# Kernel tuning notes

Measured on AMD Instinct MI355X. Metric: run time of the kernel, lower is better.

The kernel has to match this reference:

```python
import jax, jax.numpy as jnp
import numpy as np

B, L, H, NH, P = 4, 1024, 1024, 16, 2048
HD = H // NH


def setup_inputs() -> dict:
    key = jax.random.key(0)
    ks = jax.random.split(key, 6)
    x = jax.random.normal(ks[0], (B, L, H), dtype=jnp.float32)
    # torch.nn.Linear weights are [out, in]
    Wqkv = jax.random.normal(ks[1], (3 * H, H), dtype=jnp.float32) * 0.02
    bqkv = jnp.zeros((3 * H,), dtype=jnp.float32)
    Wo = jax.random.normal(ks[2], (H, H), dtype=jnp.float32) * 0.02
    bo = jnp.zeros((H,), dtype=jnp.float32)
    Er = jax.random.normal(ks[3], (NH, P, HD), dtype=jnp.float32)
    # causal mask: True where attention is disallowed (masked_fill semantics)
    mask = jnp.triu(jnp.ones((L, L), dtype=bool), k=1)
    return {"x": x, "mask": mask, "Wqkv": Wqkv, "bqkv": bqkv,
            "Wo": Wo, "bo": bo, "Er": Er}


def reference(x, mask, Wqkv, bqkv, Wo, bo, Er):
    b, l, d = x.shape
    nh, p, hd = Er.shape
    qkv = x @ Wqkv.T + bqkv                      # [b, l, 3d]
    q, k, v = jnp.split(qkv, 3, axis=-1)
    q = q.reshape(b, l, nh, hd).transpose(0, 2, 1, 3)   # [b, nh, l, hd]
    k = k.reshape(b, l, nh, hd).transpose(0, 2, 1, 3)
    v = v.reshape(b, l, nh, hd).transpose(0, 2, 1, 3)

    scores = jnp.einsum('bnlh,bnkh->bnlk', q, k) / jnp.sqrt(
        jnp.asarray(hd, dtype=x.dtype))

    # relative positions (j - i), torch negative-index wraparound -> mod p
    pos = jnp.arange(l)
    rel = (pos[None, :] - pos[:, None]) % p      # [l, l] in [0, p)
    # Equivalent to einsum('bnlh,rnlkh->bnlk', q, Er[:, rel][None]) but
    # computed as q @ Er^T over all positions then gathered (same math,
    # avoids materializing the [nh, l, l, hd] tensor).
    QEr_full = jnp.einsum('bnlh,nph->bnlp', q, Er)       # [b, nh, l, p]
    i_idx = pos[:, None]                          # broadcasts with rel
    QEr = QEr_full[:, :, i_idx, rel]              # [b, nh, l, l]

    a = scores + QEr
    a = jnp.where(mask, -jnp.inf, a)
    a = jax.nn.softmax(a, axis=-1)                # dropout: eval mode (identity)

    out = jnp.einsum('bnlk,bnkh->bnlh', a, v)     # [b, nh, l, hd]
    out = out.transpose(0, 2, 1, 3).reshape(b, l, d)
    return out @ Wo.T + bo
```

## Files before the change

### kernel.cpp

```cpp
#include <hip/hip_runtime.h>

typedef unsigned short u16;
typedef __bf16 bf16x8 __attribute__((ext_vector_type(8)));
typedef unsigned short u16x8 __attribute__((ext_vector_type(8)));
typedef unsigned short u16x4 __attribute__((ext_vector_type(4)));
typedef float f32x4 __attribute__((ext_vector_type(4)));

#define MFMA16(a, b, c) __builtin_amdgcn_mfma_f32_16x16x32_bf16((a), (b), (c), 0, 0, 0)

#define WAVE_LDS_FENCE() do { \
  asm volatile("s_waitcnt lgkmcnt(0)" ::: "memory"); \
  __builtin_amdgcn_sched_barrier(0); \
} while (0)

#define PIPE_WAIT(N) do { \
  asm volatile("s_waitcnt vmcnt(" #N ")" ::: "memory"); \
  __builtin_amdgcn_sched_barrier(0); \
  __builtin_amdgcn_s_barrier(); \
  __builtin_amdgcn_sched_barrier(0); \
} while (0)

#define GLDS(gp, lp) __builtin_amdgcn_global_load_lds( \
    (const __attribute__((address_space(1))) unsigned int*)(gp), \
    (__attribute__((address_space(3))) unsigned int*)(lp), 16, 0, 0)

__device__ __forceinline__ u16 f2b(float f) {
  unsigned u = __float_as_uint(f);
  u += 0x7fffu + ((u >> 16) & 1u);
  return (u16)(u >> 16);
}
__device__ __forceinline__ float b2f(u16 h) {
  return __uint_as_float(((unsigned)h) << 16);
}

__global__ void cvt_all(const float* __restrict__ x, u16* __restrict__ xb,
                        const float* __restrict__ w1, u16* __restrict__ w1b,
                        const float* __restrict__ w2, u16* __restrict__ w2b) {
  int i = blockIdx.x * blockDim.x + threadIdx.x;
  const float* s; u16* d; int off;
  if (i < 1048576)      { s = x;  d = xb;  off = i; }
  else if (i < 1835008) { s = w1; d = w1b; off = i - 1048576; }
  else                  { s = w2; d = w2b; off = i - 1835008; }
  float4 v = *(const float4*)(s + (size_t)off * 4);
  *(ushort4*)(d + (size_t)off * 4) = make_ushort4(f2b(v.x), f2b(v.y), f2b(v.z), f2b(v.w));
}

__global__ void build_F(const float* __restrict__ Er, u16* __restrict__ Fb) {
  int i = blockIdx.x * blockDim.x + threadIdx.x;
  int base = i * 4;
  int d = base & 63;
  int m = (base >> 6) & 1023;
  int n = base >> 16;
  int sm = (2048 - m) & 2047;
  float4 v = *(const float4*)(Er + ((size_t)(n * 2048 + sm) * 64 + d));
  *(ushort4*)(Fb + (size_t)base) = make_ushort4(f2b(v.x), f2b(v.y), f2b(v.z), f2b(v.w));
}

__global__ __launch_bounds__(256) void transpose_v(const u16* __restrict__ V, u16* __restrict__ Vt) {
  __shared__ u16 T[4096];
  const int bn = blockIdx.x, i0 = blockIdx.y * 64;
  const int t = threadIdx.x;
#pragma unroll
  for (int s = 0; s < 2; ++s) {
    int ch = t + 256 * s;
    int i = ch >> 3, c = ch & 7;
    u16x8 v = *(const u16x8*)&V[(size_t)((bn << 10) + i0 + i) * 64 + c * 8];
#pragma unroll
    for (int e = 0; e < 8; ++e) {
      int d = c * 8 + e;
      T[d * 64 + ((((i >> 3) ^ (d & 7) ^ ((d >> 3) & 7)) & 7) << 3) + (i & 7)] = v[e];
    }
  }
  __syncthreads();
#pragma unroll
  for (int s = 0; s < 2; ++s) {
    int ch = t + 256 * s;
    int d = ch >> 3, cc = ch & 7;
    u16x8 o = *(const u16x8*)&T[d * 64 + (((cc ^ (d & 7) ^ ((d >> 3) & 7)) & 7) << 3)];
    *(u16x8*)&Vt[(size_t)((bn << 6) + d) * 1024 + i0 + cc * 8] = o;
  }
}

__global__ __launch_bounds__(256) void gemm_qkv(const u16* __restrict__ A, const u16* __restrict__ Bw,
                                                const float* __restrict__ bias,
                                                u16* __restrict__ Qo, u16* __restrict__ Ko,
                                                u16* __restrict__ Vo) {
  __shared__ u16 As[3][4][128][8];
  __shared__ u16 Bs[3][4][128][8];
  const int orig = blockIdx.y * 24 + blockIdx.x;
  const int xcd = orig & 7, q = orig >> 3;
  const int mt = ((xcd >> 1) << 3) + q / 12;
  const int nt = (xcd & 1) * 12 + q % 12;
  const int m0 = mt * 128, n0 = nt * 128;
  const int t = threadIdx.x, lane = t & 63, w = t >> 6;
  const int wr = w >> 1, wc = w & 1;
  const int l16 = lane & 15, lg = lane >> 4;
  f32x4 acc[4][4] = {};
  const int r0 = t & 127, g0 = t >> 7;
  const int g1 = g0 + 2;

#define STAGE(buf, k0) do { \
    GLDS(&A[(size_t)(m0 + r0) * 1024 + (k0) + g0 * 8], &As[buf][g0][r0][0]); \
    GLDS(&A[(size_t)(m0 + r0) * 1024 + (k0) + g1 * 8], &As[buf][g1][r0][0]); \
    GLDS(&Bw[(size_t)(n0 + r0) * 1024 + (k0) + g0 * 8], &Bs[buf][g0][r0][0]); \
    GLDS(&Bw[(size_t)(n0 + r0) * 1024 + (k0) + g1 * 8], &Bs[buf][g1][r0][0]); \
  } while (0)

  STAGE(0, 0);
  STAGE(1, 32);

  int buf = 0;
  for (int kt = 0; kt < 32; ++kt) {
    if (kt < 31) PIPE_WAIT(4); else PIPE_WAIT(0);
    if (kt < 30) {
      int nb = buf + 2; if (nb >= 3) nb -= 3;
      STAGE(nb, (kt + 2) * 32);
      __builtin_amdgcn_sched_barrier(0);
    }
    bf16x8 af[4], bfr[4];
#pragma unroll
    for (int m = 0; m < 4; ++m) af[m] = *(const bf16x8*)&As[buf][lg][wr * 64 + m * 16 + l16][0];
#pragma unroll
    for (int n = 0; n < 4; ++n) bfr[n] = *(const bf16x8*)&Bs[buf][lg][wc * 64 + n * 16 + l16][0];
#pragma unroll
    for (int m = 0; m < 4; ++m)
#pragma unroll
      for (int n = 0; n < 4; ++n) acc[m][n] = MFMA16(af[m], bfr[n], acc[m][n]);
    if (++buf == 3) buf = 0;
  }
#undef STAGE

#pragma unroll
  for (int n = 0; n < 4; ++n) {
    int col = n0 + wc * 64 + n * 16 + l16;
    float bq = bias[col];
    int which = col >> 10;
    int h = col & 1023;
    int head = h >> 6, d = h & 63;
    u16* dst = which == 0 ? Qo : (which == 1 ? Ko : Vo);
    float scale = which == 1 ? 0.125f : 1.0f;
#pragma unroll
    for (int m = 0; m < 4; ++m) {
#pragma unroll
      for (int r = 0; r < 4; ++r) {
        int row = m0 + wr * 64 + m * 16 + lg * 4 + r;
        int b = row >> 10, ii = row & 1023;
        float v = (acc[m][n][r] + bq) * scale;
        dst[(size_t)(((b * 16 + head) << 10) + ii) * 64 + d] = f2b(v);
      }
    }
  }
}

__global__ __launch_bounds__(256) void gemm_out(const u16* __restrict__ A, const u16* __restrict__ Bw,
                                                const float* __restrict__ bias, float* __restrict__ Co) {
  __shared__ u16 As[3][4][128][8];
  __shared__ u16 Bs[3][4][128][8];
  const int orig = blockIdx.y * 8 + blockIdx.x;
  const int xcd = orig & 7, q = orig >> 3;
  const int mt = (xcd << 2) + (q >> 3);
  const int nt = q & 7;
  const int m0 = mt * 128, n0 = nt * 128;
  const int t = threadIdx.x, lane = t & 63, w = t >> 6;
  const int wr = w >> 1, wc = w & 1;
  const int l16 = lane & 15, lg = lane >> 4;
  f32x4 acc[4][4] = {};
  const int r0 = t & 127, g0 = t >> 7;
  const int g1 = g0 + 2;

#define STAGE(buf, k0) do { \
    GLDS(&A[(size_t)(m0 + r0) * 1024 + (k0) + g0 * 8], &As[buf][g0][r0][0]); \
    GLDS(&A[(size_t)(m0 + r0) * 1024 + (k0) + g1 * 8], &As[buf][g1][r0][0]); \
    GLDS(&Bw[(size_t)(n0 + r0) * 1024 + (k0) + g0 * 8], &Bs[buf][g0][r0][0]); \
    GLDS(&Bw[(size_t)(n0 + r0) * 1024 + (k0) + g1 * 8], &Bs[buf][g1][r0][0]); \
  } while (0)

  STAGE(0, 0);
  STAGE(1, 32);

  int buf = 0;
  for (int kt = 0; kt < 32; ++kt) {
    if (kt < 31) PIPE_WAIT(4); else PIPE_WAIT(0);
    if (kt < 30) {
      int nb = buf + 2; if (nb >= 3) nb -= 3;
      STAGE(nb, (kt + 2) * 32);
      __builtin_amdgcn_sched_barrier(0);
    }
    bf16x8 af[4], bfr[4];
#pragma unroll
    for (int m = 0; m < 4; ++m) af[m] = *(const bf16x8*)&As[buf][lg][wr * 64 + m * 16 + l16][0];
#pragma unroll
    for (int n = 0; n < 4; ++n) bfr[n] = *(const bf16x8*)&Bs[buf][lg][wc * 64 + n * 16 + l16][0];
#pragma unroll
    for (int m = 0; m < 4; ++m)
#pragma unroll
      for (int n = 0; n < 4; ++n) acc[m][n] = MFMA16(af[m], bfr[n], acc[m][n]);
    if (++buf == 3) buf = 0;
  }
#undef STAGE

#pragma unroll
  for (int n = 0; n < 4; ++n) {
    int col = n0 + wc * 64 + n * 16 + l16;
    float bq = bias[col];
#pragma unroll
    for (int m = 0; m < 4; ++m) {
#pragma unroll
      for (int r = 0; r < 4; ++r) {
        int row = m0 + wr * 64 + m * 16 + lg * 4 + r;
        Co[(size_t)row * 1024 + col] = acc[m][n][r] + bq;
      }
    }
  }
}

__global__ __launch_bounds__(256) void attn_kernel(const u16* __restrict__ Qg, const u16* __restrict__ Kg,
                                                   const u16* __restrict__ Vtg, const u16* __restrict__ Fg,
                                                   u16* __restrict__ AO) {
  __shared__ u16 Kl[4096];
  __shared__ u16 Vl[4096];
  __shared__ u16 Fl[8192];
  __shared__ u16 Bnd2[4][1024];
  __shared__ u16 Pl[4][1024];

  const int bn = blockIdx.x;
  const int b = bn >> 4, n = bn & 15;
  const int qt = 15 - (int)blockIdx.y;
  const int i0 = qt * 64;
  const int t = threadIdx.x, lane = t & 63, w = t >> 6;
  const int l16 = lane & 15, lg = lane >> 4;

  const int rr0 = t >> 3, cc0 = t & 7;
  const int rr1 = (t + 256) >> 3, cc1 = t & 7;

  bf16x8 qf[2];
  {
    const u16* qp = &Qg[(size_t)((bn << 10) + i0 + (w << 4) + l16) * 64 + lg * 8];
    qf[0] = *(const bf16x8*)qp;
    qf[1] = *(const bf16x8*)(qp + 32);
  }

  {
    int mb0 = i0 - 63;
    int h0 = 64 + rr0, h1 = 64 + rr1;
    int gm0 = mb0 + h0; gm0 = gm0 < 0 ? 0 : (gm0 > 1023 ? 1023 : gm0);
    int gm1 = mb0 + h1; gm1 = gm1 < 0 ? 0 : (gm1 > 1023 ? 1023 : gm1);
    u16x8 a = *(const u16x8*)&Fg[(size_t)((n << 10) + gm0) * 64 + cc0 * 8];
    u16x8 c = *(const u16x8*)&Fg[(size_t)((n << 10) + gm1) * 64 + cc1 * 8];
    *(u16x8*)&Fl[h0 * 64 + (((cc0 ^ (h0 & 7)) & 7) << 3)] = a;
    *(u16x8*)&Fl[h1 * 64 + (((cc1 ^ (h1 & 7)) & 7) << 3)] = c;
  }

  float mrun[4], lsum[4];
  f32x4 ao[4] = {};
#pragma unroll
  for (int r = 0; r < 4; ++r) { mrun[r] = -3.0e38f; lsum[r] = 0.0f; }

  u16x8 rk0, rk1, rv0, rv1, rf0, rf1;

#define LOAD_STAGE(jt_) do { \
    int j0_ = (jt_) * 64, mb_ = i0 - j0_ - 63; \
    rk0 = *(const u16x8*)&Kg[(size_t)((bn << 10) + j0_ + rr0) * 64 + cc0 * 8]; \
    rk1 = *(const u16x8*)&Kg[(size_t)((bn << 10) + j0_ + rr1) * 64 + cc1 * 8]; \
    rv0 = *(const u16x8*)&Vtg[(size_t)((bn << 6) + rr0) * 1024 + j0_ + cc0 * 8]; \
    rv1 = *(const u16x8*)&Vtg[(size_t)((bn << 6) + rr1) * 1024 + j0_ + cc1 * 8]; \
    int m0_ = mb_ + rr0; m0_ = m0_ < 0 ? 0 : (m0_ > 1023 ? 1023 : m0_); \
    int m1_ = mb_ + rr1; m1_ = m1_ < 0 ? 0 : (m1_ > 1023 ? 1023 : m1_); \
    rf0 = *(const u16x8*)&Fg[(size_t)((n << 10) + m0_) * 64 + cc0 * 8]; \
    rf1 = *(const u16x8*)&Fg[(size_t)((n << 10) + m1_) * 64 + cc1 * 8]; \
  } while (0)

  LOAD_STAGE(0);

  for (int jt = 0; jt <= qt; ++jt) {
    const bool diag = (jt == qt);
    const int ph = (jt & 1) << 6;

    *(u16x8*)&Kl[rr0 * 64 + (((cc0 ^ (rr0 & 7)) & 7) << 3)] = rk0;
    *(u16x8*)&Kl[rr1 * 64 + (((cc1 ^ (rr1 & 7)) & 7) << 3)] = rk1;
    *(u16x8*)&Vl[rr0 * 64 + (((cc0 ^ (rr0 & 7)) & 7) << 3)] = rv0;
    *(u16x8*)&Vl[rr1 * 64 + (((cc1 ^ (rr1 & 7)) & 7) << 3)] = rv1;
    *(u16x8*)&Fl[(rr0 ^ ph) * 64 + (((cc0 ^ (rr0 & 7)) & 7) << 3)] = rf0;
    *(u16x8*)&Fl[(rr1 ^ ph) * 64 + (((cc1 ^ (rr1 & 7)) & 7) << 3)] = rf1;
    __syncthreads();

    if (jt < qt) LOAD_STAGE(jt + 1);

    __builtin_amdgcn_s_setprio(1);
    f32x4 sc[4] = {};
#pragma unroll
    for (int kk = 0; kk < 2; ++kk)
#pragma unroll
      for (int nn = 0; nn < 4; ++nn) {
        int jr = nn * 16 + l16;
        bf16x8 kb = *(const bf16x8*)&Kl[jr * 64 + ((((lg + 4 * kk) ^ (jr & 7)) & 7) << 3)];
        sc[nn] = MFMA16(qf[kk], kb, sc[nn]);
      }
    f32x4 bb[5] = {};
#pragma unroll
    for (int kk = 0; kk < 2; ++kk)
#pragma unroll
      for (int ct = 0; ct < 5; ++ct) {
        int trow = (w << 4) + ct * 16 + l16;
        bf16x8 fb = *(const bf16x8*)&Fl[(trow ^ ph) * 64 + ((((lg + 4 * kk) ^ (trow & 7)) & 7) << 3)];
        bb[ct] = MFMA16(qf[kk], fb, bb[ct]);
      }
    __builtin_amdgcn_s_setprio(0);

#pragma unroll
    for (int ct = 0; ct < 5; ++ct)
#pragma unroll
      for (int r = 0; r < 4; ++r) {
        int il = lg * 4 + r;
        int jl = il + 63 - (ct * 16 + l16);
        if ((unsigned)jl < 64u)
          Bnd2[w][il * 64 + ((jl & 15) << 2) + (jl >> 4)] = f2b(bb[ct][r]);
      }
    WAVE_LDS_FENCE();

    float pv[4][4];
#pragma unroll
    for (int r = 0; r < 4; ++r) {
      int il = lg * 4 + r;
      u16x4 gv = *(const u16x4*)&Bnd2[w][il * 64 + (l16 << 2)];
      float stmp[4];
      float mx = -3.0e38f;
#pragma unroll
      for (int nn = 0; nn < 4; ++nn) {
        int jl = nn * 16 + l16;
        float s = sc[nn][r] + b2f(gv[nn]);
        if (diag && jl > (w << 4) + il) s = -1.0e30f;
        stmp[nn] = s;
        mx = fmaxf(mx, s);
      }
#pragma unroll
      for (int off = 1; off < 16; off <<= 1) mx = fmaxf(mx, __shfl_xor(mx, off));
      float mnew = fmaxf(mrun[r], mx);
      float scl = __expf(mrun[r] - mnew);
      float rs = 0.0f;
#pragma unroll
      for (int nn = 0; nn < 4; ++nn) {
        pv[nn][r] = __expf(stmp[nn] - mnew);
        rs += pv[nn][r];
      }
      lsum[r] = lsum[r] * scl + rs;
      mrun[r] = mnew;
#pragma unroll
      for (int nd = 0; nd < 4; ++nd) ao[nd][r] *= scl;
    }

#pragma unroll
    for (int nn = 0; nn < 4; ++nn)
#pragma unroll
      for (int r = 0; r < 4; ++r) {
        int i = lg * 4 + r, j = nn * 16 + l16;
        Pl[w][i * 64 + ((((j >> 3) ^ (i & 7)) & 7) << 3) + (j & 7)] = f2b(pv[nn][r]);
      }
    WAVE_LDS_FENCE();
    __builtin_amdgcn_s_setprio(1);
#pragma unroll
    for (int kk = 0; kk < 2; ++kk) {
      bf16x8 pa = *(const bf16x8*)&Pl[w][l16 * 64 + ((((lg + 4 * kk) ^ (l16 & 7)) & 7) << 3)];
#pragma unroll
      for (int nd = 0; nd < 4; ++nd) {
        int dr = nd * 16 + l16;
        bf16x8 vb = *(const bf16x8*)&Vl[dr * 64 + ((((lg + 4 * kk) ^ (dr & 7)) & 7) << 3)];
        ao[nd] = MFMA16(pa, vb, ao[nd]);
      }
    }
    __builtin_amdgcn_s_setprio(0);
    __syncthreads();
  }

#pragma unroll
  for (int r = 0; r < 4; ++r)
#pragma unroll
    for (int off = 1; off < 16; off <<= 1) lsum[r] += __shfl_xor(lsum[r], off);

#pragma unroll
  for (int nd = 0; nd < 4; ++nd)
#pragma unroll
    for (int r = 0; r < 4; ++r) {
      int i = i0 + (w << 4) + lg * 4 + r;
      int d = nd * 16 + l16;
      float v = ao[nd][r] / lsum[r];
      AO[(size_t)((b << 10) + i) * 1024 + n * 64 + d] = f2b(v);
    }
#undef LOAD_STAGE
}

extern "C" void kernel_launch(void* const* d_in, const int* in_sizes, int n_in,
                              void* d_out, int out_size, void* d_ws, size_t ws_size,
                              hipStream_t stream) {
  (void)in_sizes; (void)n_in; (void)out_size; (void)ws_size;
  const float* x    = (const float*)d_in[0];
  const float* Wqkv = (const float*)d_in[2];
  const float* bqkv = (const float*)d_in[3];
  const float* Wo   = (const float*)d_in[4];
  const float* bo   = (const float*)d_in[5];
  const float* Er   = (const float*)d_in[6];
  float* out = (float*)d_out;

  char* p = (char*)d_ws;
  u16* xb    = (u16*)p; p += (size_t)4096 * 1024 * 2;
  u16* wqkvb = (u16*)p; p += (size_t)3072 * 1024 * 2;
  u16* wob   = (u16*)p; p += (size_t)1024 * 1024 * 2;
  u16* Fb    = (u16*)p; p += (size_t)16 * 1024 * 64 * 2;
  u16* Qb    = (u16*)p; p += (size_t)64 * 1024 * 64 * 2;
  u16* Kb    = (u16*)p; p += (size_t)64 * 1024 * 64 * 2;
  u16* Vb    = (u16*)p; p += (size_t)64 * 1024 * 64 * 2;
  u16* Vtb   = (u16*)p; p += (size_t)64 * 1024 * 64 * 2;
  u16* AO    = (u16*)p; p += (size_t)4096 * 1024 * 2;

  cvt_all<<<8192, 256, 0, stream>>>(x, xb, Wqkv, wqkvb, Wo, wob);
  build_F<<<1024, 256, 0, stream>>>(Er, Fb);
  gemm_qkv<<<dim3(24, 32), 256, 0, stream>>>(xb, wqkvb, bqkv, Qb, Kb, Vb);
  transpose_v<<<dim3(64, 16), 256, 0, stream>>>(Vb, Vtb);
  attn_kernel<<<dim3(64, 16), 256, 0, stream>>>(Qb, Kb, Vtb, Fb, AO);
  gemm_out<<<dim3(8, 32), 256, 0, stream>>>(AO, wob, bo, out);
}
```

Measured before the change: 153.0 us.

## Fuse V transpose into QKV GEMM epilogue and add lazy softmax rescaling

The QKV GEMM epilogue now writes V directly in transposed [head, d, seq] layout using 4-element vector stores, which removes the separate transpose_v kernel launch and its extra round trip through global memory. The attention softmax also skips rescaling the running output and sum whenever the new row max stays within a threshold of the running max, so the max update and accumulator scaling are avoided most of the time. Trade-offs: the transposed V stores are narrow and strided, and exponents can grow up to e^8 before renormalisation, which is still safe in fp32 accumulators.

Result: slower. 156.4 us (+2.2%).

```diff
diff --git a/kernel.cpp b/kernel.cpp
--- a/kernel.cpp
+++ b/kernel.cpp
@@ -56,35 +56,10 @@
   *(ushort4*)(Fb + (size_t)base) = make_ushort4(f2b(v.x), f2b(v.y), f2b(v.z), f2b(v.w));
 }
 
-__global__ __launch_bounds__(256) void transpose_v(const u16* __restrict__ V, u16* __restrict__ Vt) {
-  __shared__ u16 T[4096];
-  const int bn = blockIdx.x, i0 = blockIdx.y * 64;
-  const int t = threadIdx.x;
-#pragma unroll
-  for (int s = 0; s < 2; ++s) {
-    int ch = t + 256 * s;
-    int i = ch >> 3, c = ch & 7;
-    u16x8 v = *(const u16x8*)&V[(size_t)((bn << 10) + i0 + i) * 64 + c * 8];
-#pragma unroll
-    for (int e = 0; e < 8; ++e) {
-      int d = c * 8 + e;
-      T[d * 64 + ((((i >> 3) ^ (d & 7) ^ ((d >> 3) & 7)) & 7) << 3) + (i & 7)] = v[e];
-    }
-  }
-  __syncthreads();
-#pragma unroll
-  for (int s = 0; s < 2; ++s) {
-    int ch = t + 256 * s;
-    int d = ch >> 3, cc = ch & 7;
-    u16x8 o = *(const u16x8*)&T[d * 64 + (((cc ^ (d & 7) ^ ((d >> 3) & 7)) & 7) << 3)];
-    *(u16x8*)&Vt[(size_t)((bn << 6) + d) * 1024 + i0 + cc * 8] = o;
-  }
-}
-
 __global__ __launch_bounds__(256) void gemm_qkv(const u16* __restrict__ A, const u16* __restrict__ Bw,
                                                 const float* __restrict__ bias,
                                                 u16* __restrict__ Qo, u16* __restrict__ Ko,
-                                                u16* __restrict__ Vo) {
+                                                u16* __restrict__ Vt) {
   __shared__ u16 As[3][4][128][8];
   __shared__ u16 Bs[3][4][128][8];
   const int orig = blockIdx.y * 24 + blockIdx.x;
@@ -137,16 +112,27 @@
     int which = col >> 10;
     int h = col & 1023;
     int head = h >> 6, d = h & 63;
-    u16* dst = which == 0 ? Qo : (which == 1 ? Ko : Vo);
-    float scale = which == 1 ? 0.125f : 1.0f;
-#pragma unroll
-    for (int m = 0; m < 4; ++m) {
-#pragma unroll
-      for (int r = 0; r < 4; ++r) {
-        int row = m0 + wr * 64 + m * 16 + lg * 4 + r;
+    if (which == 2) {
+#pragma unroll
+      for (int m = 0; m < 4; ++m) {
+        int row = m0 + wr * 64 + m * 16 + lg * 4;
         int b = row >> 10, ii = row & 1023;
-        float v = (acc[m][n][r] + bq) * scale;
-        dst[(size_t)(((b * 16 + head) << 10) + ii) * 64 + d] = f2b(v);
+        u16x4 o;
+#pragma unroll
+        for (int r = 0; r < 4; ++r) o[r] = f2b(acc[m][n][r] + bq);
+        *(u16x4*)&Vt[(size_t)(((b * 16 + head) << 6) + d) * 1024 + ii] = o;
+      }
+    } else {
+      u16* dst = which == 0 ? Qo : Ko;
+      float scale = which == 1 ? 0.125f : 1.0f;
+#pragma unroll
+      for (int m = 0; m < 4; ++m) {
+#pragma unroll
+        for (int r = 0; r < 4; ++r) {
+          int row = m0 + wr * 64 + m * 16 + lg * 4 + r;
+          int b = row >> 10, ii = row & 1023;
+          dst[(size_t)(((b * 16 + head) << 10) + ii) * 64 + d] = f2b((acc[m][n][r] + bq) * scale);
+        }
       }
     }
   }
@@ -335,18 +321,28 @@
       }
 #pragma unroll
       for (int off = 1; off < 16; off <<= 1) mx = fmaxf(mx, __shfl_xor(mx, off));
-      float mnew = fmaxf(mrun[r], mx);
-      float scl = __expf(mrun[r] - mnew);
-      float rs = 0.0f;
-#pragma unroll
-      for (int nn = 0; nn < 4; ++nn) {
-        pv[nn][r] = __expf(stmp[nn] - mnew);
-        rs += pv[nn][r];
-      }
-      lsum[r] = lsum[r] * scl + rs;
-      mrun[r] = mnew;
-#pragma unroll
-      for (int nd = 0; nd < 4; ++nd) ao[nd][r] *= scl;
+      if (mx <= mrun[r] + 8.0f) {
+        float rs = 0.0f;
+#pragma unroll
+        for (int nn = 0; nn < 4; ++nn) {
+          pv[nn][r] = __expf(stmp[nn] - mrun[r]);
+          rs += pv[nn][r];
+        }
+        lsum[r] += rs;
+      } else {
+        float mnew = fmaxf(mrun[r], mx);
+        float scl = __expf(mrun[r] - mnew);
+        float rs = 0.0f;
+#pragma unroll
+        for (int nn = 0; nn < 4; ++nn) {
+          pv[nn][r] = __expf(stmp[nn] - mnew);
+          rs += pv[nn][r];
+        }
+        lsum[r] = lsum[r] * scl + rs;
+        mrun[r] = mnew;
+#pragma unroll
+        for (int nd = 0; nd < 4; ++nd) ao[nd][r] *= scl;
+      }
     }
 
 #pragma unroll
@@ -408,14 +404,12 @@
   u16* Fb    = (u16*)p; p += (size_t)16 * 1024 * 64 * 2;
   u16* Qb    = (u16*)p; p += (size_t)64 * 1024 * 64 * 2;
   u16* Kb    = (u16*)p; p += (size_t)64 * 1024 * 64 * 2;
-  u16* Vb    = (u16*)p; p += (size_t)64 * 1024 * 64 * 2;
   u16* Vtb   = (u16*)p; p += (size_t)64 * 1024 * 64 * 2;
   u16* AO    = (u16*)p; p += (size_t)4096 * 1024 * 2;
 
   cvt_all<<<8192, 256, 0, stream>>>(x, xb, Wqkv, wqkvb, Wo, wob);
   build_F<<<1024, 256, 0, stream>>>(Er, Fb);
-  gemm_qkv<<<dim3(24, 32), 256, 0, stream>>>(xb, wqkvb, bqkv, Qb, Kb, Vb);
-  transpose_v<<<dim3(64, 16), 256, 0, stream>>>(Vb, Vtb);
+  gemm_qkv<<<dim3(24, 32), 256, 0, stream>>>(xb, wqkvb, bqkv, Qb, Kb, Vtb);
   attn_kernel<<<dim3(64, 16), 256, 0, stream>>>(Qb, Kb, Vtb, Fb, AO);
   gemm_out<<<dim3(8, 32), 256, 0, stream>>>(AO, wob, bo, out);
 }
```
